# Kernel optimization log

Measured on AMD Instinct MI355X. Metric: run time of the kernel, lower is better.

Reference implementation:

```python
import jax, jax.numpy as jnp
import numpy as np

K, OUT, IN = 4, 4096, 4096
B, S = 2, 2048

def setup_inputs() -> dict:
    key = jax.random.key(0)
    k1, k2, k3 = jax.random.split(key, 3)
    x = jax.random.normal(k1, (B, S, IN), dtype=jnp.float32)
    alphas = jax.random.normal(k2, (K,), dtype=jnp.float32)
    # binary bases in {-1, +1}, stored as int8 like the torch buffer
    bases = (jax.random.randint(k3, (K, OUT, IN), 0, 2) * 2 - 1).astype(jnp.int8)
    return {"x": x, "alphas": alphas, "bases": bases}

def reference(x, alphas, bases):
    # W_q = sum_i alphas[i] * bases[i]  -> [out, in]
    W_q = jnp.einsum('k,koi->oi', alphas, bases.astype(x.dtype))
    # y = x @ W_q.T  -> [B, S, out]
    return jnp.einsum('bsi,oi->bso', x, W_q)
```

## Files before the change

### kernel.cpp

```cpp
#include <hip/hip_runtime.h>
#include <hip/hip_bf16.h>
#include <stdint.h>

#define DIM_M 4096
#define DIM_N 4096
#define DIM_K 4096
#define BASE_STRIDE (DIM_N * DIM_K)

#define RS 40

typedef __bf16 bf16x8 __attribute__((ext_vector_type(8)));
typedef float floatx16 __attribute__((ext_vector_type(16)));
typedef unsigned short ushort8 __attribute__((ext_vector_type(8)));

__device__ __forceinline__ unsigned short f2bf(float f) {
    uint32_t u = __float_as_uint(f);
    uint32_t r = (u + 0x7FFFu + ((u >> 16) & 1u)) >> 16;
    return (unsigned short)r;
}

__global__ __launch_bounds__(256) void prep_kernel(
        const int* __restrict__ bases, const float* __restrict__ alphas,
        const float* __restrict__ x,
        unsigned short* __restrict__ Wb, unsigned short* __restrict__ Xb) {
    const int bid = blockIdx.x;
    if (bid < 8192) {
        const long e = ((long)bid * 256 + threadIdx.x) * 8;
        const float a0 = alphas[0], a1 = alphas[1], a2 = alphas[2], a3 = alphas[3];
        const int4 p0 = *(const int4*)(bases + e);
        const int4 p1 = *(const int4*)(bases + e + 4);
        const int4 q0 = *(const int4*)(bases + BASE_STRIDE + e);
        const int4 q1 = *(const int4*)(bases + BASE_STRIDE + e + 4);
        const int4 r0 = *(const int4*)(bases + 2L * BASE_STRIDE + e);
        const int4 r1 = *(const int4*)(bases + 2L * BASE_STRIDE + e + 4);
        const int4 s0 = *(const int4*)(bases + 3L * BASE_STRIDE + e);
        const int4 s1 = *(const int4*)(bases + 3L * BASE_STRIDE + e + 4);
        ushort8 o;
        o[0] = f2bf(a0 * p0.x + a1 * q0.x + a2 * r0.x + a3 * s0.x);
        o[1] = f2bf(a0 * p0.y + a1 * q0.y + a2 * r0.y + a3 * s0.y);
        o[2] = f2bf(a0 * p0.z + a1 * q0.z + a2 * r0.z + a3 * s0.z);
        o[3] = f2bf(a0 * p0.w + a1 * q0.w + a2 * r0.w + a3 * s0.w);
        o[4] = f2bf(a0 * p1.x + a1 * q1.x + a2 * r1.x + a3 * s1.x);
        o[5] = f2bf(a0 * p1.y + a1 * q1.y + a2 * r1.y + a3 * s1.y);
        o[6] = f2bf(a0 * p1.z + a1 * q1.z + a2 * r1.z + a3 * s1.z);
        o[7] = f2bf(a0 * p1.w + a1 * q1.w + a2 * r1.w + a3 * s1.w);
        *(ushort8*)(Wb + e) = o;
    } else {
        const long e = ((long)(bid - 8192) * 256 + threadIdx.x) * 8;
        const float4 v0 = *(const float4*)(x + e);
        const float4 v1 = *(const float4*)(x + e + 4);
        ushort8 o;
        o[0] = f2bf(v0.x); o[1] = f2bf(v0.y); o[2] = f2bf(v0.z); o[3] = f2bf(v0.w);
        o[4] = f2bf(v1.x); o[5] = f2bf(v1.y); o[6] = f2bf(v1.z); o[7] = f2bf(v1.w);
        *(ushort8*)(Xb + e) = o;
    }
}

__global__ __launch_bounds__(256, 4) void gemm_bt_kernel(
        const unsigned short* __restrict__ A, const unsigned short* __restrict__ Bt,
        float* __restrict__ C) {
    __shared__ unsigned short sA[2 * 128 * RS];
    __shared__ unsigned short sB[2 * 128 * RS];

    const int t = threadIdx.x;
    const int wave = t >> 6, lane = t & 63;
    const int wm = (wave >> 1) * 64;
    const int wn = (wave & 1) * 64;
    const int l31 = lane & 31, g = lane >> 5;

    const int mBase = blockIdx.y * 128;
    const int nBase = blockIdx.x * 128;

    const int srow = t >> 2;
    const int sch = (t & 3) * 8;
    const unsigned short* gA0 = A + (size_t)(mBase + srow) * DIM_K + sch;
    const unsigned short* gA1 = gA0 + (size_t)64 * DIM_K;
    const unsigned short* gB0 = Bt + (size_t)(nBase + srow) * DIM_K + sch;
    const unsigned short* gB1 = gB0 + (size_t)64 * DIM_K;
    const int lo0 = srow * RS + sch;
    const int lo1 = (64 + srow) * RS + sch;

    const int arow = (wm + l31) * RS;
    const int brow = (wn + l31) * RS;

    floatx16 acc[2][2] = {};

    ushort8 rA0 = *(const ushort8*)gA0;
    ushort8 rA1 = *(const ushort8*)gA1;
    ushort8 rB0 = *(const ushort8*)gB0;
    ushort8 rB1 = *(const ushort8*)gB1;
    gA0 += 32; gA1 += 32; gB0 += 32; gB1 += 32;
    *(ushort8*)(sA + lo0) = rA0;
    *(ushort8*)(sA + lo1) = rA1;
    *(ushort8*)(sB + lo0) = rB0;
    *(ushort8*)(sB + lo1) = rB1;
    __syncthreads();

    int p = 0;
    for (int kt = 0; kt < DIM_K; kt += 32) {
        const bool more = (kt + 32) < DIM_K;
        if (more) {
            rA0 = *(const ushort8*)gA0;
            rA1 = *(const ushort8*)gA1;
            rB0 = *(const ushort8*)gB0;
            rB1 = *(const ushort8*)gB1;
            gA0 += 32; gA1 += 32; gB0 += 32; gB1 += 32;
        }

        const unsigned short* bufA = sA + p * (128 * RS);
        const unsigned short* bufB = sB + p * (128 * RS);
        bf16x8 a[2][2], b[2][2];
#pragma unroll
        for (int i = 0; i < 2; i++) {
            a[i][0] = *(const bf16x8*)(bufA + arow + i * 32 * RS + (0 + g) * 8);
            a[i][1] = *(const bf16x8*)(bufA + arow + i * 32 * RS + (2 + g) * 8);
        }
#pragma unroll
        for (int j = 0; j < 2; j++) {
            b[j][0] = *(const bf16x8*)(bufB + brow + j * 32 * RS + (0 + g) * 8);
            b[j][1] = *(const bf16x8*)(bufB + brow + j * 32 * RS + (2 + g) * 8);
        }

#pragma unroll
        for (int h = 0; h < 2; h++)
#pragma unroll
            for (int i = 0; i < 2; i++)
#pragma unroll
                for (int j = 0; j < 2; j++)
                    acc[i][j] = __builtin_amdgcn_mfma_f32_32x32x16_bf16(
                        a[i][h], b[j][h], acc[i][j], 0, 0, 0);

        if (more) {
            unsigned short* wA = sA + (p ^ 1) * (128 * RS);
            unsigned short* wB = sB + (p ^ 1) * (128 * RS);
            *(ushort8*)(wA + lo0) = rA0;
            *(ushort8*)(wA + lo1) = rA1;
            *(ushort8*)(wB + lo0) = rB0;
            *(ushort8*)(wB + lo1) = rB1;
        }
        __syncthreads();
        p ^= 1;
    }

#pragma unroll
    for (int i = 0; i < 2; i++) {
#pragma unroll
        for (int j = 0; j < 2; j++) {
#pragma unroll
            for (int r = 0; r < 16; r++) {
                const int row = mBase + wm + i * 32 + (r & 3) + 8 * (r >> 2) + 4 * g;
                const int col = nBase + wn + j * 32 + l31;
                C[(size_t)row * DIM_N + col] = acc[i][j][r];
            }
        }
    }
}

__global__ __launch_bounds__(256) void naive_kernel(
        const float* __restrict__ x, const float* __restrict__ alphas,
        const int* __restrict__ bases, float* __restrict__ out) {
    const long o = (long)blockIdx.x * 256 + threadIdx.x;
    const int m = (int)(o >> 12), n = (int)(o & 4095);
    const float a0 = alphas[0], a1 = alphas[1], a2 = alphas[2], a3 = alphas[3];
    const float* xr = x + (long)m * DIM_K;
    const int* b0 = bases + (long)n * DIM_K;
    const int* b1 = b0 + BASE_STRIDE;
    const int* b2 = b1 + BASE_STRIDE;
    const int* b3 = b2 + BASE_STRIDE;
    float acc = 0.f;
    for (int i = 0; i < DIM_K; i++) {
        float w = a0 * b0[i] + a1 * b1[i] + a2 * b2[i] + a3 * b3[i];
        acc += xr[i] * w;
    }
    out[o] = acc;
}

extern "C" void kernel_launch(void* const* d_in, const int* in_sizes, int n_in,
                              void* d_out, int out_size, void* d_ws, size_t ws_size,
                              hipStream_t stream) {
    const float* x      = (const float*)d_in[0];
    const float* alphas = (const float*)d_in[1];
    const int*   bases  = (const int*)d_in[2];
    float* out = (float*)d_out;

    const size_t need = (size_t)2 * DIM_N * DIM_K + (size_t)2 * DIM_M * DIM_K;
    if (ws_size >= need) {
        unsigned short* Wb = (unsigned short*)d_ws;
        unsigned short* Xb = (unsigned short*)d_ws + (size_t)DIM_N * DIM_K;
        prep_kernel<<<16384, 256, 0, stream>>>(bases, alphas, x, Wb, Xb);
        gemm_bt_kernel<<<dim3(DIM_N / 128, DIM_M / 128), 256, 0, stream>>>(Xb, Wb, out);
    } else {
        naive_kernel<<<(DIM_M * DIM_N) / 256, 256, 0, stream>>>(x, alphas, bases, out);
    }
}
```

Baseline: 587.6 us.

## Rewrite bf16 GEMM as 256x256 tile with direct-to-LDS loads and ping-pong schedule

Replaces the 128x128 four-wave GEMM with a 256x256 tile computed by 8 waves. Global data now goes straight into LDS via global_load_lds, using an XOR-swizzled layout in place of row padding. The K loop runs as an explicitly interleaved schedule of LDS reads, async stages, barriers and prioritized MFMA bursts, with vmcnt waits placed by hand. This is meant to raise arithmetic intensity and overlap memory with matrix math. The cost is 128KB of LDS per block, many barriers, and hand-tuned wait counts that are fragile to get right.

```diff
diff --git a/kernel.cpp b/kernel.cpp
--- a/kernel.cpp
+++ b/kernel.cpp
@@ -6,8 +6,7 @@
 #define DIM_N 4096
 #define DIM_K 4096
 #define BASE_STRIDE (DIM_N * DIM_K)
-
-#define RS 40
+#define NT (DIM_K / 64)
 
 typedef __bf16 bf16x8 __attribute__((ext_vector_type(8)));
 typedef float floatx16 __attribute__((ext_vector_type(16)));
@@ -56,101 +55,126 @@
     }
 }
 
-__global__ __launch_bounds__(256, 4) void gemm_bt_kernel(
+#define MFMA32 __builtin_amdgcn_mfma_f32_32x32x16_bf16
+#define BAR()   __builtin_amdgcn_s_barrier()
+#define PRIO1() __builtin_amdgcn_s_setprio(1)
+#define PRIO0() __builtin_amdgcn_s_setprio(0)
+
+__device__ __forceinline__ void stage_half(const unsigned short* __restrict__ gb,
+        int grow0, int kbase, unsigned short* ld, int wave, int lane) {
+#pragma unroll
+    for (int r = 0; r < 2; ++r) {
+        const int row = wave * 16 + r * 8 + (lane >> 3);
+        const int ch  = (lane & 7) ^ (row & 7);
+        const unsigned short* g = gb + (size_t)(grow0 + row) * DIM_K + kbase + ch * 8;
+        unsigned short* d = ld + (wave * 16 + r * 8) * 64;
+        __builtin_amdgcn_global_load_lds(
+            (const __attribute__((address_space(1))) unsigned int*)((const void*)g),
+            (__attribute__((address_space(3))) unsigned int*)((void*)d), 16, 0, 0);
+    }
+}
+
+#define DS_A(LD, MI, SLOT)                                                        \
+    do { _Pragma("unroll") for (int k = 0; k < 4; ++k)                            \
+        a[SLOT][k] = *(const bf16x8*)((LD) + ((MI) * 32 + l31) * 64 + cko[k]);    \
+    } while (0)
+#define DS_B(LD, NH, SLOT)                                                        \
+    do { _Pragma("unroll") for (int k = 0; k < 4; ++k)                            \
+        b[SLOT][k] = *(const bf16x8*)((LD) + (nloc + (NH) * 32 + l31) * 64 + cko[k]); \
+    } while (0)
+#define MM2(MI0, MI1, NH, SB)                                                     \
+    do { _Pragma("unroll") for (int k = 0; k < 4; ++k) {                          \
+        acc[MI0][NH] = MFMA32(a[0][k], b[SB][k], acc[MI0][NH], 0, 0, 0);          \
+        acc[MI1][NH] = MFMA32(a[1][k], b[SB][k], acc[MI1][NH], 0, 0, 0);          \
+    } } while (0)
+
+__global__ __launch_bounds__(512, 2) void gemm_bt_kernel(
         const unsigned short* __restrict__ A, const unsigned short* __restrict__ Bt,
         float* __restrict__ C) {
-    __shared__ unsigned short sA[2 * 128 * RS];
-    __shared__ unsigned short sB[2 * 128 * RS];
+    __shared__ __align__(16) unsigned short lds[2][2][2][128 * 64];
 
     const int t = threadIdx.x;
     const int wave = t >> 6, lane = t & 63;
-    const int wm = (wave >> 1) * 64;
-    const int wn = (wave & 1) * 64;
-    const int l31 = lane & 31, g = lane >> 5;
-
-    const int mBase = blockIdx.y * 128;
-    const int nBase = blockIdx.x * 128;
-
-    const int srow = t >> 2;
-    const int sch = (t & 3) * 8;
-    const unsigned short* gA0 = A + (size_t)(mBase + srow) * DIM_K + sch;
-    const unsigned short* gA1 = gA0 + (size_t)64 * DIM_K;
-    const unsigned short* gB0 = Bt + (size_t)(nBase + srow) * DIM_K + sch;
-    const unsigned short* gB1 = gB0 + (size_t)64 * DIM_K;
-    const int lo0 = srow * RS + sch;
-    const int lo1 = (64 + srow) * RS + sch;
-
-    const int arow = (wm + l31) * RS;
-    const int brow = (wn + l31) * RS;
-
-    floatx16 acc[2][2] = {};
-
-    ushort8 rA0 = *(const ushort8*)gA0;
-    ushort8 rA1 = *(const ushort8*)gA1;
-    ushort8 rB0 = *(const ushort8*)gB0;
-    ushort8 rB1 = *(const ushort8*)gB1;
-    gA0 += 32; gA1 += 32; gB0 += 32; gB1 += 32;
-    *(ushort8*)(sA + lo0) = rA0;
-    *(ushort8*)(sA + lo1) = rA1;
-    *(ushort8*)(sB + lo0) = rB0;
-    *(ushort8*)(sB + lo1) = rB1;
-    __syncthreads();
-
-    int p = 0;
-    for (int kt = 0; kt < DIM_K; kt += 32) {
-        const bool more = (kt + 32) < DIM_K;
+    const int l31 = lane & 31, g32 = lane >> 5;
+    const int wm = wave >> 2;
+    const int wn = wave & 3;
+    const int nloc = (wn & 1) * 64;
+
+    const int mBase = blockIdx.y * 256;
+    const int nBase = blockIdx.x * 256;
+
+    const unsigned short* LA0 = &lds[0][0][wm][0];
+    const unsigned short* LA1 = &lds[1][0][wm][0];
+    const unsigned short* LB0 = &lds[0][1][wn >> 1][0];
+    const unsigned short* LB1 = &lds[1][1][wn >> 1][0];
+
+    int cko[4];
+#pragma unroll
+    for (int k = 0; k < 4; ++k) cko[k] = ((k * 2 + g32) ^ (l31 & 7)) * 8;
+
+    floatx16 acc[4][2] = {};
+    bf16x8 a[2][4], b[2][4];
+
+    stage_half(A,  mBase + 0,   0,  &lds[0][0][0][0], wave, lane);
+    stage_half(A,  mBase + 128, 0,  &lds[0][0][1][0], wave, lane);
+    stage_half(Bt, nBase + 0,   0,  &lds[0][1][0][0], wave, lane);
+    stage_half(Bt, nBase + 128, 0,  &lds[0][1][1][0], wave, lane);
+    stage_half(Bt, nBase + 0,   64, &lds[1][1][0][0], wave, lane);
+    stage_half(Bt, nBase + 128, 64, &lds[1][1][1][0], wave, lane);
+    stage_half(A,  mBase + 0,   64, &lds[1][0][0][0], wave, lane);
+    asm volatile("s_waitcnt vmcnt(6)" ::: "memory");
+    BAR();
+
+    for (int i = 0; i < NT / 2; ++i) {
+        const bool more = (i < NT / 2 - 1);
+        const int t1k = (2 * i + 1) * 64;
+        const int t2k = (2 * i + 2) * 64;
+        const int t3k = (2 * i + 3) * 64;
+
+        DS_A(LA0, 0, 0); DS_A(LA0, 1, 1); DS_B(LB0, 0, 0);
+        stage_half(A, mBase + 128, t1k, &lds[1][0][1][0], wave, lane);
+        BAR(); PRIO1(); MM2(0, 1, 0, 0); PRIO0(); BAR();
+        DS_B(LB0, 1, 1);
+        BAR(); PRIO1(); MM2(0, 1, 1, 1); PRIO0(); BAR();
+        DS_A(LA0, 2, 0); DS_A(LA0, 3, 1);
+        if (more) stage_half(Bt, nBase + 0, t2k, &lds[0][1][0][0], wave, lane);
+        BAR(); PRIO1(); MM2(2, 3, 1, 1); PRIO0(); BAR();
         if (more) {
-            rA0 = *(const ushort8*)gA0;
-            rA1 = *(const ushort8*)gA1;
-            rB0 = *(const ushort8*)gB0;
-            rB1 = *(const ushort8*)gB1;
-            gA0 += 32; gA1 += 32; gB0 += 32; gB1 += 32;
+            stage_half(Bt, nBase + 128, t2k, &lds[0][1][1][0], wave, lane);
+            stage_half(A,  mBase + 0,   t2k, &lds[0][0][0][0], wave, lane);
+            asm volatile("s_waitcnt vmcnt(6)" ::: "memory");
+        } else {
+            asm volatile("s_waitcnt vmcnt(0)" ::: "memory");
         }
-
-        const unsigned short* bufA = sA + p * (128 * RS);
-        const unsigned short* bufB = sB + p * (128 * RS);
-        bf16x8 a[2][2], b[2][2];
-#pragma unroll
-        for (int i = 0; i < 2; i++) {
-            a[i][0] = *(const bf16x8*)(bufA + arow + i * 32 * RS + (0 + g) * 8);
-            a[i][1] = *(const bf16x8*)(bufA + arow + i * 32 * RS + (2 + g) * 8);
+        BAR(); PRIO1(); MM2(2, 3, 0, 0); PRIO0(); BAR();
+
+        DS_A(LA1, 0, 0); DS_A(LA1, 1, 1); DS_B(LB1, 0, 0);
+        if (more) stage_half(A, mBase + 128, t2k, &lds[0][0][1][0], wave, lane);
+        BAR(); PRIO1(); MM2(0, 1, 0, 0); PRIO0(); BAR();
+        DS_B(LB1, 1, 1);
+        BAR(); PRIO1(); MM2(0, 1, 1, 1); PRIO0(); BAR();
+        DS_A(LA1, 2, 0); DS_A(LA1, 3, 1);
+        if (more) stage_half(Bt, nBase + 0, t3k, &lds[1][1][0][0], wave, lane);
+        BAR(); PRIO1(); MM2(2, 3, 1, 1); PRIO0(); BAR();
+        if (more) {
+            stage_half(Bt, nBase + 128, t3k, &lds[1][1][1][0], wave, lane);
+            stage_half(A,  mBase + 0,   t3k, &lds[1][0][0][0], wave, lane);
+            asm volatile("s_waitcnt vmcnt(6)" ::: "memory");
+        } else {
+            asm volatile("s_waitcnt vmcnt(0)" ::: "memory");
         }
-#pragma unroll
-        for (int j = 0; j < 2; j++) {
-            b[j][0] = *(const bf16x8*)(bufB + brow + j * 32 * RS + (0 + g) * 8);
-            b[j][1] = *(const bf16x8*)(bufB + brow + j * 32 * RS + (2 + g) * 8);
-        }
-
-#pragma unroll
-        for (int h = 0; h < 2; h++)
-#pragma unroll
-            for (int i = 0; i < 2; i++)
-#pragma unroll
-                for (int j = 0; j < 2; j++)
-                    acc[i][j] = __builtin_amdgcn_mfma_f32_32x32x16_bf16(
-                        a[i][h], b[j][h], acc[i][j], 0, 0, 0);
-
-        if (more) {
-            unsigned short* wA = sA + (p ^ 1) * (128 * RS);
-            unsigned short* wB = sB + (p ^ 1) * (128 * RS);
-            *(ushort8*)(wA + lo0) = rA0;
-            *(ushort8*)(wA + lo1) = rA1;
-            *(ushort8*)(wB + lo0) = rB0;
-            *(ushort8*)(wB + lo1) = rB1;
-        }
-        __syncthreads();
-        p ^= 1;
-    }
-
-#pragma unroll
-    for (int i = 0; i < 2; i++) {
-#pragma unroll
-        for (int j = 0; j < 2; j++) {
-#pragma unroll
-            for (int r = 0; r < 16; r++) {
-                const int row = mBase + wm + i * 32 + (r & 3) + 8 * (r >> 2) + 4 * g;
-                const int col = nBase + wn + j * 32 + l31;
-                C[(size_t)row * DIM_N + col] = acc[i][j][r];
+        BAR(); PRIO1(); MM2(2, 3, 0, 0); PRIO0(); BAR();
+    }
+
+#pragma unroll
+    for (int mi = 0; mi < 4; ++mi) {
+#pragma unroll
+        for (int nh = 0; nh < 2; ++nh) {
+#pragma unroll
+            for (int r = 0; r < 16; ++r) {
+                const int row = mBase + wm * 128 + mi * 32 + (r & 3) + 8 * (r >> 2) + 4 * g32;
+                const int col = nBase + wn * 64 + nh * 32 + l31;
+                C[(size_t)row * DIM_N + col] = acc[mi][nh][r];
             }
         }
     }
@@ -188,7 +212,7 @@
         unsigned short* Wb = (unsigned short*)d_ws;
         unsigned short* Xb = (unsigned short*)d_ws + (size_t)DIM_N * DIM_K;
         prep_kernel<<<16384, 256, 0, stream>>>(bases, alphas, x, Wb, Xb);
-        gemm_bt_kernel<<<dim3(DIM_N / 128, DIM_M / 128), 256, 0, stream>>>(Xb, Wb, out);
+        gemm_bt_kernel<<<dim3(DIM_N / 256, DIM_M / 256), 512, 0, stream>>>(Xb, Wb, out);
     } else {
         naive_kernel<<<(DIM_M * DIM_N) / 256, 256, 0, stream>>>(x, alphas, bases, out);
     }
```

Result: faster. 542.3 us (-7.7%).
